# Kernel tuning notes

Hardware: AMD Instinct MI355X
Metric: run time of the kernel (lower is better)

## Reference

```python
import jax, jax.numpy as jnp
import numpy as np

B, T, HS, WS = 4, 16, 32, 64          # batch, time, lat, lon
D_MODEL, N_HEADS = 256, 8
E = D_MODEL // N_HEADS                 # 32 per-head dim
MODES = [8, 8, 16]
F_LAST = WS // 2 + 1                   # 33 rfft bins on last dim
M_LAST = MODES[-1]                     # 16 kept rfft bins
M_PANEL = MODES[0] * MODES[1]          # 64 kept (T,HS) panel modes


def _sym_indexes(shape):
    # faithful numpy port of get_symmetry_index_in_fft_pannel
    shape = np.array(shape)
    idx = np.stack([t.flatten() for t in np.meshgrid(*[range(s) for s in shape])])
    idx2 = (-idx) % shape[:, None]
    fftshift = (idx + shape[:, None] // 2) % shape[:, None]
    center = (shape[:, None] - 1) / 2
    order = np.argsort(np.linalg.norm(fftshift - center, axis=0))
    idx = idx[:, order]
    idx2 = idx2[:, order]
    return np.ravel_multi_index(idx, shape), np.ravel_multi_index(idx2, shape)


def _picked_panel():
    # lowest-frequency mode selection honoring Hermitian pairing
    i1, i2 = _sym_indexes((T, HS))
    picked = []
    for a, b in zip(i1, i2):
        if a in picked or b in picked:
            continue
        picked.append(a)
        if len(picked) == M_PANEL:
            break
    return np.array(picked, dtype=np.int32), i1.astype(np.int32), i2.astype(np.int32)


def setup_inputs() -> dict:
    key = jax.random.key(0)
    ks = jax.random.split(key, 12)
    sl = 1.0 / np.float32(np.sqrt(D_MODEL))
    sw = np.float32(0.02)
    panel, s1, s2 = _picked_panel()
    return {
        "x": jax.random.normal(ks[0], (B, T, HS, WS, D_MODEL), jnp.float32),
        "Wq": jax.random.normal(ks[1], (D_MODEL, D_MODEL), jnp.float32) * sl,
        "bq": jnp.zeros((D_MODEL,), jnp.float32),
        "Wk": jax.random.normal(ks[2], (D_MODEL, D_MODEL), jnp.float32) * sl,
        "bk": jnp.zeros((D_MODEL,), jnp.float32),
        "Wv": jax.random.normal(ks[3], (D_MODEL, D_MODEL), jnp.float32) * sl,
        "bv": jnp.zeros((D_MODEL,), jnp.float32),
        "Wo": jax.random.normal(ks[4], (D_MODEL, D_MODEL), jnp.float32) * sl,
        "bo": jnp.zeros((D_MODEL,), jnp.float32),
        "w_real": jax.random.normal(ks[5], (N_HEADS, E, E, M_PANEL, M_LAST), jnp.float32) * sw,
        "w_imag": jax.random.normal(ks[6], (N_HEADS, E, E, M_PANEL, M_LAST), jnp.float32) * sw,
        "panel_idx": jnp.asarray(panel),
        "sym_idx1": jnp.asarray(s1),
        "sym_idx2": jnp.asarray(s2),
    }


def reference(x, Wq, bq, Wk, bk, Wv, bv, Wo, bo, w_real, w_imag,
              panel_idx, sym_idx1, sym_idx2):
    # QKV projections (the torch layer computes all three; FourierBlockN uses q)
    q = (x @ Wq + bq).reshape(B, T, HS, WS, N_HEADS, E).transpose(0, 4, 5, 1, 2, 3)
    _k = (x @ Wk + bk)
    _v = (x @ Wv + bv)
    # rfftn over the spacetime dims -> (B,H,E,T,HS,F_LAST)
    x_ft = jnp.fft.rfftn(q, axes=(-3, -2, -1)).reshape(B, N_HEADS, E, T * HS, F_LAST)
    # gather selected frequency modes
    x_sel = x_ft[:, :, :, panel_idx, :M_LAST]                    # (B,H,E,Mp,Ml)
    w = w_real + 1j * w_imag                                      # (H,E,E,Mp,Ml)
    out_sel = jnp.einsum('bhipf,hiopf->bhopf', x_sel, w)
    out_ft = jnp.zeros_like(x_ft)
    out_ft = out_ft.at[:, :, :, panel_idx, :M_LAST].set(out_sel)
    # canonical_fft_freq: enforce Hermitian symmetry on the (T,HS) panel
    out_ft = out_ft.at[:, :, :, sym_idx1, :].set(
        (out_ft[:, :, :, sym_idx1, :] + jnp.conj(out_ft[:, :, :, sym_idx2, :])) * 0.5)
    out_ft = out_ft.reshape(B, N_HEADS, E, T, HS, F_LAST)
    o = jnp.fft.irfftn(out_ft, s=(T, HS, WS), axes=(-3, -2, -1))  # (B,H,E,T,HS,WS)
    o = o.transpose(0, 3, 4, 5, 1, 2).reshape(B, T, HS, WS, N_HEADS * E)
    return o @ Wo + bo
```

## Files before the change

kernel.cpp:

```cpp
#include <hip/hip_runtime.h>
#include <hip/hip_bf16.h>
#include <cmath>

#define BB 4
#define TT 16
#define HH 32
#define WW 64
#define DD 256
#define NHEAD 8
#define EE 32
#define MP 64
#define ML 16
#define SPAT 32768
#define S2D 512

constexpr size_t OFF_FTRE = 0;
constexpr size_t OFF_FTIM = 1024;
constexpr size_t OFF_FHRE = 2048;
constexpr size_t OFF_FHIM = 4096;
constexpr size_t OFF_CW   = 6144;
constexpr size_t OFF_W64I = 7168;
constexpr size_t OFF_W16  = 9216;
constexpr size_t OFF_FHT  = 9728;
constexpr size_t OFF_GB   = 16384;
constexpr size_t OFF_FW   = OFF_GB + 8388608;
constexpr size_t OFF_X    = OFF_FW + 16777216;
constexpr size_t OFF_V    = OFF_X + 2097152;
constexpr size_t OFF_WT   = OFF_V + 2097152;

typedef short short8 __attribute__((ext_vector_type(8)));
typedef float f32x4 __attribute__((ext_vector_type(4)));

static __device__ __forceinline__ unsigned short f2bf(float x) {
  union { float f; unsigned u; } v; v.f = x;
  unsigned r = v.u + 0x7fffu + ((v.u >> 16) & 1u);
  return (unsigned short)(r >> 16);
}

static __device__ __forceinline__ void gl_lds16(const void* g, void* l) {
  __builtin_amdgcn_global_load_lds((const __attribute__((address_space(1))) void*)g,
                                   (__attribute__((address_space(3))) void*)l, 16, 0, 0);
}

static __device__ __forceinline__ void xcd_tile_dg(int flat, int& tile, int& dg) {
  int w8 = flat >> 3, xl = flat & 7;
  tile = ((w8 >> 2) << 3) | xl;
  dg = w8 & 3;
}

__global__ __launch_bounds__(256) void k0_tables(const int* __restrict__ panel, float* __restrict__ tab) {
  __shared__ int kt[MP], kh[MP];
  int tid = threadIdx.x;
  if (tid < MP) { int s = panel[tid]; kt[tid] = s >> 5; kh[tid] = s & 31; }
  __syncthreads();
  const double PI2 = 6.283185307179586476925286766559;
  for (int i = tid; i < 1024; i += 256) {
    int p = i >> 4, t = i & 15;
    double a = -PI2 * (double)((t * kt[p]) & 15) / 16.0;
    tab[OFF_FTRE + i] = (float)cos(a);
    tab[OFF_FTIM + i] = (float)sin(a);
  }
  for (int i = tid; i < 2048; i += 256) {
    int p = i >> 5, hs = i & 31;
    double a = -PI2 * (double)((hs * kh[p]) & 31) / 32.0;
    tab[OFF_FHRE + i] = (float)cos(a);
    tab[OFF_FHIM + i] = (float)sin(a);
  }
  for (int i = tid; i < 1024; i += 256) {
    int f = i >> 6, wsx = i & 63;
    double a = PI2 * (double)((f * wsx) & 63) / 64.0;
    tab[OFF_CW + i] = (f == 0) ? (1.0f / 64.0f) : (float)(2.0 * cos(a) / 64.0);
  }
  for (int i = tid; i < 2048; i += 256) {
    int wsx = i >> 5, f2 = i & 31; int f = f2 >> 1;
    double a = -PI2 * (double)((wsx * f) & 63) / 64.0;
    tab[OFF_W64I + i] = (f2 & 1) ? (float)sin(a) : (float)cos(a);
  }
  if (tid < 256) {
    int t = tid >> 4, k = tid & 15;
    double a = -PI2 * (double)((t * k) & 15) / 16.0;
    tab[OFF_W16 + 2 * tid]     = (float)cos(a);
    tab[OFF_W16 + 2 * tid + 1] = (float)sin(a);
  }
  for (int i = tid; i < 2048; i += 256) {
    int hs = i >> 6, p = i & 63;
    double a = -PI2 * (double)((hs * kh[p]) & 31) / 32.0;
    tab[OFF_FHT + 2 * i]     = (float)cos(a);
    tab[OFF_FHT + 2 * i + 1] = (float)sin(a);
  }
}

__global__ __launch_bounds__(256) void conv_w(const float* __restrict__ Wq, const float* __restrict__ Wo,
                                              unsigned short* __restrict__ wqt, unsigned short* __restrict__ wot) {
  __shared__ float tile[32][33];
  const float* src = blockIdx.z ? Wo : Wq;
  unsigned short* dst = blockIdx.z ? wot : wqt;
  int k0 = blockIdx.x * 32, d0 = blockIdx.y * 32;
  int tx = threadIdx.x & 31, r4 = threadIdx.x >> 5;
  #pragma unroll
  for (int it = 0; it < 4; it++) {
    int row = r4 + it * 8;
    tile[row][tx] = src[(size_t)(k0 + row) * 256 + d0 + tx];
  }
  __syncthreads();
  #pragma unroll
  for (int it = 0; it < 4; it++) {
    int row = r4 + it * 8;
    dst[(size_t)(d0 + row) * 256 + k0 + tx] = f2bf(tile[tx][row]);
  }
}

__global__ __launch_bounds__(256) void k1f3(const float* __restrict__ x,
                                            const unsigned short* __restrict__ wqt,
                                            const float* __restrict__ bq,
                                            const float* __restrict__ tabp,
                                            float* __restrict__ Fwg) {
  __shared__ char smem[32768];
  char*  Al = smem;
  char*  Bl = smem + 16384;
  float* QL = (float*)smem;
  float* WL = (float*)(smem + 24576);
  int tile, dg;
  xcd_tile_dg(blockIdx.x, tile, dg);
  int d0 = dg << 6;
  int b = tile >> 8, st = tile & 255;
  int sp0 = st << 7;
  int tid = threadIdx.x;
  int lane = tid & 63, w = tid >> 6;
  int l15 = lane & 15, kg = lane >> 4;
  int swz = (l15 & 7) << 4;
  for (int i = tid; i < 2048; i += 256) WL[i] = tabp[OFF_W64I + i];
  f32x4 acc[2][4];
  #pragma unroll
  for (int mi = 0; mi < 2; mi++)
    #pragma unroll
    for (int ni = 0; ni < 4; ni++) acc[mi][ni] = (f32x4){0.f, 0.f, 0.f, 0.f};
  const float* xbase = x + ((size_t)b * 32768 + sp0) * 256;
  const char* Bbase = (const char*)(wqt + (size_t)d0 * 256);
  for (int k0 = 0; k0 < 256; k0 += 64) {
    #pragma unroll
    for (int it = 0; it < 2; it++) {
      int o = it * 4096 + tid * 16;
      int row = o >> 7, cb = o & 127;
      gl_lds16(Bbase + (size_t)row * 512 + k0 * 2 + (cb ^ ((row & 7) << 4)), Bl + o);
    }
    #pragma unroll
    for (int it = 0; it < 4; it++) {
      int idx = it * 256 + tid;
      int row = idx >> 3, g8 = idx & 7;
      const float* src = xbase + (size_t)row * 256 + k0 + g8 * 8;
      float4 a4 = *reinterpret_cast<const float4*>(src);
      float4 b4 = *reinterpret_cast<const float4*>(src + 4);
      short8 v;
      v[0] = (short)f2bf(a4.x); v[1] = (short)f2bf(a4.y); v[2] = (short)f2bf(a4.z); v[3] = (short)f2bf(a4.w);
      v[4] = (short)f2bf(b4.x); v[5] = (short)f2bf(b4.y); v[6] = (short)f2bf(b4.z); v[7] = (short)f2bf(b4.w);
      int byteoff = (row * 128 + g8 * 16) ^ ((row & 7) << 4);
      *reinterpret_cast<short8*>(Al + byteoff) = v;
    }
    __syncthreads();
    #pragma unroll
    for (int ks = 0; ks < 2; ks++) {
      int koff = (ks * 64 + kg * 16) ^ swz;
      short8 af[2], bfr[4];
      #pragma unroll
      for (int mi = 0; mi < 2; mi++)
        af[mi] = *reinterpret_cast<const short8*>(Al + (w * 32 + mi * 16 + l15) * 128 + koff);
      #pragma unroll
      for (int ni = 0; ni < 4; ni++)
        bfr[ni] = *reinterpret_cast<const short8*>(Bl + (ni * 16 + l15) * 128 + koff);
      #pragma unroll
      for (int mi = 0; mi < 2; mi++)
        #pragma unroll
        for (int ni = 0; ni < 4; ni++)
          acc[mi][ni] = __builtin_amdgcn_mfma_f32_16x16x32_bf16(af[mi], bfr[ni], acc[mi][ni], 0, 0, 0);
    }
    __syncthreads();
  }
  #pragma unroll
  for (int sh = 0; sh < 2; sh++) {
    if ((w >> 1) == sh) {
      #pragma unroll
      for (int ni = 0; ni < 4; ni++) {
        float bqv = bq[d0 + ni * 16 + l15];
        #pragma unroll
        for (int mi = 0; mi < 2; mi++) {
          f32x4 vv = acc[mi][ni];
          int m = (w & 1) * 32 + mi * 16 + kg * 4;
          #pragma unroll
          for (int j = 0; j < 4; j++)
            QL[(m + j) * 68 + ni * 16 + l15] = vv[j] + bqv;
        }
      }
    }
    __syncthreads();
    {
      int dp = tid >> 3, f2q = tid & 7;
      f32x4 a0 = (f32x4){0.f, 0.f, 0.f, 0.f};
      f32x4 a1 = (f32x4){0.f, 0.f, 0.f, 0.f};
      const float* qbase = QL + dp * 2;
      const float* wbase = WL + f2q * 4;
      #pragma unroll 8
      for (int wsx = 0; wsx < 64; wsx++) {
        float2 q = *reinterpret_cast<const float2*>(qbase + wsx * 68);
        f32x4 wv = *reinterpret_cast<const f32x4*>(wbase + wsx * 32);
        a0 += wv * q.x;
        a1 += wv * q.y;
      }
      int sgl = st * 2 + sh;
      size_t g0 = ((size_t)(b * 512 + sgl) * 256 + d0 + dp * 2) * 32 + f2q * 4;
      *reinterpret_cast<f32x4*>(&Fwg[g0]) = a0;
      *reinterpret_cast<f32x4*>(&Fwg[g0 + 32]) = a1;
    }
    if (sh == 0) __syncthreads();
  }
}

__global__ __launch_bounds__(512) void k3f(const float* __restrict__ Fwg, const float* __restrict__ tabp,
                                           const int* __restrict__ panel, float* __restrict__ X) {
  __shared__ float2 Floc[8192];
  __shared__ float2 fhT[32][64];
  __shared__ float2 W16L[16][16];
  __shared__ int ktl[64];
  int bd = blockIdx.x; int b = bd >> 8; int d = bd & 255;
  int tid = threadIdx.x;
  if (tid < 256) W16L[tid >> 4][tid & 15] = reinterpret_cast<const float2*>(tabp + OFF_W16)[tid];
  for (int i = tid; i < 2048; i += 512) fhT[i >> 6][i & 63] = reinterpret_cast<const float2*>(tabp + OFF_FHT)[i];
  if (tid < 64) ktl[tid] = panel[tid] >> 5;
  {
    const char* gb = (const char*)Fwg;
    #pragma unroll
    for (int r = 0; r < 8; r++) {
      int o = r * 8192 + tid * 16;
      int s = o >> 7; int c16 = (o >> 4) & 7;
      size_t gaddr = ((size_t)(b * 512 + s) * 256 + d) * 128 + (size_t)c16 * 16;
      gl_lds16(gb + gaddr, (char*)Floc + o);
    }
  }
  __syncthreads();
  int hs = tid >> 4, f = tid & 15;
  float2 v[16];
  #pragma unroll
  for (int t = 0; t < 16; t++) v[t] = Floc[(t * 32 + hs) * 16 + f];
  float2 a[16];
  #pragma unroll
  for (int k = 0; k < 16; k++) a[k] = make_float2(0.f, 0.f);
  #pragma unroll
  for (int t = 0; t < 16; t++) {
    float2 vv = v[t];
    #pragma unroll
    for (int k = 0; k < 16; k++) {
      float2 w = W16L[t][k];
      a[k].x += w.x * vv.x - w.y * vv.y;
      a[k].y += w.x * vv.y + w.y * vv.x;
    }
  }
  #pragma unroll
  for (int k = 0; k < 16; k++) Floc[(k * 32 + hs) * 16 + f] = a[k];
  __syncthreads();
  int p2 = tid >> 4;
  float2 res[2];
  #pragma unroll
  for (int half = 0; half < 2; half++) {
    int p = p2 + half * 32;
    int kt = ktl[p];
    float ar = 0.f, ai = 0.f;
    #pragma unroll 8
    for (int h = 0; h < 32; h++) {
      float2 e = fhT[h][p];
      float2 u = Floc[(kt * 32 + h) * 16 + f];
      ar += u.x * e.x - u.y * e.y;
      ai += u.x * e.y + u.y * e.x;
    }
    res[half] = make_float2(ar, ai);
  }
  float2* Xo = reinterpret_cast<float2*>(X) + (size_t)bd * 1024;
  Xo[p2 * 16 + f] = res[0];
  Xo[(p2 + 32) * 16 + f] = res[1];
}

__global__ __launch_bounds__(512) void k3b_mix(const float* __restrict__ X, const float* __restrict__ wreal,
                                               const float* __restrict__ wimag, float* __restrict__ V) {
  __shared__ float2 xs[4][32][16];
  int h = blockIdx.x >> 6;
  int p = blockIdx.x & 63;
  int tid = threadIdx.x;
  const float2* Xv = reinterpret_cast<const float2*>(X);
  for (int i = tid; i < 2048; i += 512) {
    int b = i >> 9, ii = (i >> 4) & 31, f = i & 15;
    xs[b][ii][f] = Xv[((size_t)(b * 256 + h * 32 + ii) * MP + p) * ML + f];
  }
  __syncthreads();
  int o = tid >> 4, f = tid & 15;
  float accr[4] = {0, 0, 0, 0}, acci[4] = {0, 0, 0, 0};
  for (int i = 0; i < 32; i++) {
    size_t wofs = ((((size_t)h * 32 + i) * 32 + o) * MP + p) * ML + f;
    float wr = wreal[wofs], wi = wimag[wofs];
    #pragma unroll
    for (int b = 0; b < 4; b++) {
      float2 xv = xs[b][i][f];
      accr[b] += xv.x * wr - xv.y * wi;
      acci[b] += xv.x * wi + xv.y * wr;
    }
  }
  #pragma unroll
  for (int b = 0; b < 4; b++)
    reinterpret_cast<float2*>(V)[((size_t)(b * 256 + h * 32 + o) * MP + p) * ML + f] =
        make_float2(accr[b], acci[b]);
}

__global__ __launch_bounds__(256) void k4a_inv(const float* __restrict__ V, const float* __restrict__ tabp,
                                               float* __restrict__ gbuf) {
  __shared__ float2 vl[64][16];
  __shared__ float2 ft[64][16];
  __shared__ float2 fh[64][32];
  int bd = blockIdx.x;
  int tid = threadIdx.x;
  const float2* Vv = reinterpret_cast<const float2*>(V) + (size_t)bd * MP * ML;
  for (int i = tid; i < 1024; i += 256) {
    vl[i >> 4][i & 15] = Vv[i];
    ft[i >> 4][i & 15] = make_float2(tabp[OFF_FTRE + i], tabp[OFF_FTIM + i]);
  }
  for (int i = tid; i < 2048; i += 256) fh[i >> 5][i & 31] = make_float2(tabp[OFF_FHRE + i], tabp[OFF_FHIM + i]);
  __syncthreads();
  float g0[16], g1[16];
  #pragma unroll
  for (int f = 0; f < 16; f++) { g0[f] = 0.f; g1[f] = 0.f; }
  int s0 = tid * 2;
  int t0 = s0 >> 5, hs0 = s0 & 31;
  int t1 = (s0 + 1) >> 5, hs1 = (s0 + 1) & 31;
  for (int p = 0; p < 64; p++) {
    float2 et0 = ft[p][t0], eh0 = fh[p][hs0];
    float2 et1 = ft[p][t1], eh1 = fh[p][hs1];
    float er0 = et0.x * eh0.x - et0.y * eh0.y;
    float ei0 = et0.x * eh0.y + et0.y * eh0.x;
    float er1 = et1.x * eh1.x - et1.y * eh1.y;
    float ei1 = et1.x * eh1.y + et1.y * eh1.x;
    #pragma unroll
    for (int f = 0; f < 16; f++) {
      float2 v = vl[p][f];
      g0[f] += v.x * er0 + v.y * ei0;
      g1[f] += v.x * er1 + v.y * ei1;
    }
  }
  float4* gb = reinterpret_cast<float4*>(gbuf + (size_t)bd * 8192 + (size_t)s0 * 16);
  #pragma unroll
  for (int q = 0; q < 4; q++)
    gb[q] = make_float4(g0[q * 4] * (1.f / 512.f), g0[q * 4 + 1] * (1.f / 512.f),
                        g0[q * 4 + 2] * (1.f / 512.f), g0[q * 4 + 3] * (1.f / 512.f));
  #pragma unroll
  for (int q = 0; q < 4; q++)
    gb[4 + q] = make_float4(g1[q * 4] * (1.f / 512.f), g1[q * 4 + 1] * (1.f / 512.f),
                            g1[q * 4 + 2] * (1.f / 512.f), g1[q * 4 + 3] * (1.f / 512.f));
}

__global__ __launch_bounds__(256) void k4b_cos(const float* __restrict__ gbuf, const float* __restrict__ tabp,
                                               unsigned short* __restrict__ ob) {
  __shared__ float Gs[256][17];
  __shared__ float cwL[16][64];
  int s = blockIdx.x, b = blockIdx.y;
  int tid = threadIdx.x;
  for (int i = tid; i < 4096; i += 256) {
    int c = i >> 4, f = i & 15;
    Gs[c][f] = gbuf[(size_t)(b * 256 + c) * 8192 + s * 16 + f];
  }
  for (int i = tid; i < 1024; i += 256) cwL[i >> 6][i & 63] = tabp[OFF_CW + i];
  __syncthreads();
  int c0 = (tid & 63) * 4, wsg = tid >> 6;
  float gv[4][16];
  #pragma unroll
  for (int j = 0; j < 4; j++)
    #pragma unroll
    for (int f = 0; f < 16; f++) gv[j][f] = Gs[c0 + j][f];
  for (int wsi = 0; wsi < 16; wsi++) {
    int wsx = wsg * 16 + wsi;
    float a0 = 0.f, a1 = 0.f, a2 = 0.f, a3 = 0.f;
    #pragma unroll
    for (int f = 0; f < 16; f++) {
      float cwv = cwL[f][wsx];
      a0 += gv[0][f] * cwv; a1 += gv[1][f] * cwv; a2 += gv[2][f] * cwv; a3 += gv[3][f] * cwv;
    }
    ushort4 u;
    u.x = f2bf(a0); u.y = f2bf(a1); u.z = f2bf(a2); u.w = f2bf(a3);
    *reinterpret_cast<ushort4*>(&ob[((size_t)b * SPAT + (size_t)s * 64 + wsx) * 256 + c0]) = u;
  }
}

__global__ __launch_bounds__(256) void k5_mfma(const unsigned short* __restrict__ ob,
                                               const unsigned short* __restrict__ wot,
                                               const float* __restrict__ bo, float* __restrict__ out) {
  __shared__ char smem[34816];
  unsigned short* Al = (unsigned short*)smem;
  unsigned short* Bl = (unsigned short*)(smem + 16384);
  float* OL = (float*)smem;
  int tile, dg;
  xcd_tile_dg(blockIdx.x, tile, dg);
  int b = tile >> 8, sp0 = (tile & 255) << 7, d0 = dg << 6;
  int tid = threadIdx.x;
  int lane = tid & 63, w = tid >> 6;
  int l15 = lane & 15, kg = lane >> 4;
  int swz = (l15 & 7) << 4;
  f32x4 acc[2][4];
  #pragma unroll
  for (int mi = 0; mi < 2; mi++)
    #pragma unroll
    for (int ni = 0; ni < 4; ni++) acc[mi][ni] = (f32x4){0.f, 0.f, 0.f, 0.f};
  const char* Abase = (const char*)(ob + ((size_t)b * 32768 + sp0) * 256);
  const char* Bbase = (const char*)(wot + (size_t)d0 * 256);
  for (int k0 = 0; k0 < 256; k0 += 64) {
    #pragma unroll
    for (int it = 0; it < 2; it++) {
      int o = tid * 16 + it * 4096 + 16384;
      int ol = o - 16384;
      int row = ol >> 7, cb = ol & 127;
      int scb = cb ^ ((row & 7) << 4);
      gl_lds16(Bbase + (size_t)row * 512 + k0 * 2 + scb, smem + o);
    }
    #pragma unroll
    for (int it = 0; it < 4; it++) {
      int o = tid * 16 + it * 4096;
      int row = o >> 7, cb = o & 127;
      int scb = cb ^ ((row & 7) << 4);
      gl_lds16(Abase + (size_t)row * 512 + k0 * 2 + scb, (char*)Al + o);
    }
    __syncthreads();
    #pragma unroll
    for (int ks = 0; ks < 2; ks++) {
      int koff = (ks * 64 + kg * 16) ^ swz;
      short8 af[2], bfr[4];
      #pragma unroll
      for (int mi = 0; mi < 2; mi++)
        af[mi] = *(const short8*)((const char*)Al + (w * 32 + mi * 16 + l15) * 128 + koff);
      #pragma unroll
      for (int ni = 0; ni < 4; ni++)
        bfr[ni] = *(const short8*)((const char*)Bl + (ni * 16 + l15) * 128 + koff);
      #pragma unroll
      for (int mi = 0; mi < 2; mi++)
        #pragma unroll
        for (int ni = 0; ni < 4; ni++)
          acc[mi][ni] = __builtin_amdgcn_mfma_f32_16x16x32_bf16(af[mi], bfr[ni], acc[mi][ni], 0, 0, 0);
    }
    __syncthreads();
  }
  #pragma unroll
  for (int ni = 0; ni < 4; ni++) {
    float bov = bo[d0 + ni * 16 + l15];
    #pragma unroll
    for (int mi = 0; mi < 2; mi++) {
      f32x4 v = acc[mi][ni];
      int m = w * 32 + mi * 16 + kg * 4;
      #pragma unroll
      for (int j = 0; j < 4; j++)
        OL[(m + j) * 68 + ni * 16 + l15] = v[j] + bov;
    }
  }
  __syncthreads();
  int f4 = tid & 15, r0 = tid >> 4;
  #pragma unroll
  for (int r = 0; r < 8; r++) {
    int m = r * 16 + r0;
    float4 val = *reinterpret_cast<const float4*>(&OL[m * 68 + f4 * 4]);
    *reinterpret_cast<float4*>(&out[((size_t)b * SPAT + sp0 + m) * 256 + d0 + f4 * 4]) = val;
  }
}

extern "C" void kernel_launch(void* const* d_in, const int* in_sizes, int n_in,
                              void* d_out, int out_size, void* d_ws, size_t ws_size,
                              hipStream_t stream) {
  const float* x  = (const float*)d_in[0];
  const float* Wq = (const float*)d_in[1];
  const float* bq = (const float*)d_in[2];
  const float* Wo = (const float*)d_in[7];
  const float* bo = (const float*)d_in[8];
  const float* wr = (const float*)d_in[9];
  const float* wi = (const float*)d_in[10];
  const int* panel = (const int*)d_in[11];
  float* wsf = (float*)d_ws;
  float* out = (float*)d_out;

  float*          gbuf = wsf + OFF_GB;
  unsigned short* obb  = (unsigned short*)(wsf + OFF_FW);
  unsigned short* wqt  = (unsigned short*)(wsf + OFF_WT);
  unsigned short* wot  = wqt + 65536;

  k0_tables<<<dim3(1), dim3(256), 0, stream>>>(panel, wsf);
  conv_w<<<dim3(8, 8, 2), dim3(256), 0, stream>>>(Wq, Wo, wqt, wot);
  k1f3<<<dim3(4096), dim3(256), 0, stream>>>(x, wqt, bq, wsf, wsf + OFF_FW);
  k3f<<<dim3(1024), dim3(512), 0, stream>>>(wsf + OFF_FW, wsf, panel, wsf + OFF_X);
  k3b_mix<<<dim3(512), dim3(512), 0, stream>>>(wsf + OFF_X, wr, wi, wsf + OFF_V);
  k4a_inv<<<dim3(1024), dim3(256), 0, stream>>>(wsf + OFF_V, wsf, gbuf);
  k4b_cos<<<dim3(512, 4), dim3(256), 0, stream>>>(gbuf, wsf, obb);
  k5_mfma<<<dim3(4096), dim3(256), 0, stream>>>(obb, wot, bo, out);
}
```

Baseline: 331.4 us.

## Preload full Wq slice to LDS and load A fragments directly from global

```diff
diff --git a/kernel.cpp b/kernel.cpp
--- a/kernel.cpp
+++ b/kernel.cpp
@@ -115,11 +115,10 @@
                                             const float* __restrict__ bq,
                                             const float* __restrict__ tabp,
                                             float* __restrict__ Fwg) {
-  __shared__ char smem[32768];
-  char*  Al = smem;
-  char*  Bl = smem + 16384;
+  __shared__ char smem[40960];
+  char*  Bl = smem;
   float* QL = (float*)smem;
-  float* WL = (float*)(smem + 24576);
+  float* WL = (float*)(smem + 32768);
   int tile, dg;
   xcd_tile_dg(blockIdx.x, tile, dg);
   int d0 = dg << 6;
@@ -130,52 +129,50 @@
   int l15 = lane & 15, kg = lane >> 4;
   int swz = (l15 & 7) << 4;
   for (int i = tid; i < 2048; i += 256) WL[i] = tabp[OFF_W64I + i];
+  {
+    const char* Bbase = (const char*)(wqt + (size_t)d0 * 256);
+    #pragma unroll
+    for (int it = 0; it < 8; it++) {
+      int o = it * 4096 + tid * 16;
+      int row = o >> 9, cb = o & 511;
+      gl_lds16(Bbase + (size_t)row * 512 + (cb ^ ((row & 7) << 4)), Bl + o);
+    }
+  }
+  __syncthreads();
   f32x4 acc[2][4];
   #pragma unroll
   for (int mi = 0; mi < 2; mi++)
     #pragma unroll
     for (int ni = 0; ni < 4; ni++) acc[mi][ni] = (f32x4){0.f, 0.f, 0.f, 0.f};
   const float* xbase = x + ((size_t)b * 32768 + sp0) * 256;
-  const char* Bbase = (const char*)(wqt + (size_t)d0 * 256);
   for (int k0 = 0; k0 < 256; k0 += 64) {
     #pragma unroll
-    for (int it = 0; it < 2; it++) {
-      int o = it * 4096 + tid * 16;
-      int row = o >> 7, cb = o & 127;
-      gl_lds16(Bbase + (size_t)row * 512 + k0 * 2 + (cb ^ ((row & 7) << 4)), Bl + o);
-    }
-    #pragma unroll
-    for (int it = 0; it < 4; it++) {
-      int idx = it * 256 + tid;
-      int row = idx >> 3, g8 = idx & 7;
-      const float* src = xbase + (size_t)row * 256 + k0 + g8 * 8;
-      float4 a4 = *reinterpret_cast<const float4*>(src);
-      float4 b4 = *reinterpret_cast<const float4*>(src + 4);
-      short8 v;
-      v[0] = (short)f2bf(a4.x); v[1] = (short)f2bf(a4.y); v[2] = (short)f2bf(a4.z); v[3] = (short)f2bf(a4.w);
-      v[4] = (short)f2bf(b4.x); v[5] = (short)f2bf(b4.y); v[6] = (short)f2bf(b4.z); v[7] = (short)f2bf(b4.w);
-      int byteoff = (row * 128 + g8 * 16) ^ ((row & 7) << 4);
-      *reinterpret_cast<short8*>(Al + byteoff) = v;
-    }
-    __syncthreads();
-    #pragma unroll
     for (int ks = 0; ks < 2; ks++) {
-      int koff = (ks * 64 + kg * 16) ^ swz;
-      short8 af[2], bfr[4];
-      #pragma unroll
-      for (int mi = 0; mi < 2; mi++)
-        af[mi] = *reinterpret_cast<const short8*>(Al + (w * 32 + mi * 16 + l15) * 128 + koff);
+      int ke = k0 + ks * 32 + kg * 8;
+      short8 af[2];
+      #pragma unroll
+      for (int mi = 0; mi < 2; mi++) {
+        const float* p = xbase + (size_t)(w * 32 + mi * 16 + l15) * 256 + ke;
+        float4 lo = *reinterpret_cast<const float4*>(p);
+        float4 hi = *reinterpret_cast<const float4*>(p + 4);
+        short8 v;
+        v[0] = (short)f2bf(lo.x); v[1] = (short)f2bf(lo.y); v[2] = (short)f2bf(lo.z); v[3] = (short)f2bf(lo.w);
+        v[4] = (short)f2bf(hi.x); v[5] = (short)f2bf(hi.y); v[6] = (short)f2bf(hi.z); v[7] = (short)f2bf(hi.w);
+        af[mi] = v;
+      }
+      int koff = (k0 * 2 + ks * 64 + kg * 16) ^ swz;
+      short8 bfr[4];
       #pragma unroll
       for (int ni = 0; ni < 4; ni++)
-        bfr[ni] = *reinterpret_cast<const short8*>(Bl + (ni * 16 + l15) * 128 + koff);
+        bfr[ni] = *reinterpret_cast<const short8*>(Bl + (size_t)(ni * 16 + l15) * 512 + koff);
       #pragma unroll
       for (int mi = 0; mi < 2; mi++)
         #pragma unroll
         for (int ni = 0; ni < 4; ni++)
           acc[mi][ni] = __builtin_amdgcn_mfma_f32_16x16x32_bf16(af[mi], bfr[ni], acc[mi][ni], 0, 0, 0);
     }
-    __syncthreads();
-  }
+  }
+  __syncthreads();
   #pragma unroll
   for (int sh = 0; sh < 2; sh++) {
     if ((w >> 1) == sh) {
```

Measured after the change: 361.2 us. 1.09x slower.

## Split k3f frequency dimension into two halves to halve LDS footprint

Applied to the files above, without the earlier changes.

```diff
diff --git a/kernel.cpp b/kernel.cpp
--- a/kernel.cpp
+++ b/kernel.cpp
@@ -217,7 +217,7 @@
 
 __global__ __launch_bounds__(512) void k3f(const float* __restrict__ Fwg, const float* __restrict__ tabp,
                                            const int* __restrict__ panel, float* __restrict__ X) {
-  __shared__ float2 Floc[8192];
+  __shared__ float2 Floc[4096];
   __shared__ float2 fhT[32][64];
   __shared__ float2 W16L[16][16];
   __shared__ int ktl[64];
@@ -226,56 +226,55 @@
   if (tid < 256) W16L[tid >> 4][tid & 15] = reinterpret_cast<const float2*>(tabp + OFF_W16)[tid];
   for (int i = tid; i < 2048; i += 512) fhT[i >> 6][i & 63] = reinterpret_cast<const float2*>(tabp + OFF_FHT)[i];
   if (tid < 64) ktl[tid] = panel[tid] >> 5;
-  {
-    const char* gb = (const char*)Fwg;
-    #pragma unroll
-    for (int r = 0; r < 8; r++) {
-      int o = r * 8192 + tid * 16;
-      int s = o >> 7; int c16 = (o >> 4) & 7;
-      size_t gaddr = ((size_t)(b * 512 + s) * 256 + d) * 128 + (size_t)c16 * 16;
-      gl_lds16(gb + gaddr, (char*)Floc + o);
-    }
-  }
-  __syncthreads();
-  int hs = tid >> 4, f = tid & 15;
-  float2 v[16];
-  #pragma unroll
-  for (int t = 0; t < 16; t++) v[t] = Floc[(t * 32 + hs) * 16 + f];
-  float2 a[16];
-  #pragma unroll
-  for (int k = 0; k < 16; k++) a[k] = make_float2(0.f, 0.f);
-  #pragma unroll
-  for (int t = 0; t < 16; t++) {
-    float2 vv = v[t];
-    #pragma unroll
-    for (int k = 0; k < 16; k++) {
-      float2 w = W16L[t][k];
-      a[k].x += w.x * vv.x - w.y * vv.y;
-      a[k].y += w.x * vv.y + w.y * vv.x;
-    }
-  }
-  #pragma unroll
-  for (int k = 0; k < 16; k++) Floc[(k * 32 + hs) * 16 + f] = a[k];
-  __syncthreads();
-  int p2 = tid >> 4;
-  float2 res[2];
-  #pragma unroll
-  for (int half = 0; half < 2; half++) {
-    int p = p2 + half * 32;
-    int kt = ktl[p];
-    float ar = 0.f, ai = 0.f;
-    #pragma unroll 8
-    for (int h = 0; h < 32; h++) {
-      float2 e = fhT[h][p];
-      float2 u = Floc[(kt * 32 + h) * 16 + f];
-      ar += u.x * e.x - u.y * e.y;
-      ai += u.x * e.y + u.y * e.x;
-    }
-    res[half] = make_float2(ar, ai);
-  }
-  float2* Xo = reinterpret_cast<float2*>(X) + (size_t)bd * 1024;
-  Xo[p2 * 16 + f] = res[0];
-  Xo[(p2 + 32) * 16 + f] = res[1];
+  #pragma unroll
+  for (int fh = 0; fh < 2; fh++) {
+    {
+      const char* gb = (const char*)Fwg;
+      #pragma unroll
+      for (int r = 0; r < 4; r++) {
+        int o = r * 8192 + tid * 16;
+        int s = o >> 6; int c16 = (o >> 4) & 3;
+        size_t gaddr = ((size_t)(b * 512 + s) * 256 + d) * 128 + (size_t)fh * 64 + (size_t)c16 * 16;
+        gl_lds16(gb + gaddr, (char*)Floc + o);
+      }
+    }
+    __syncthreads();
+    int f = tid & 7, hs = (tid >> 3) & 31, rep = tid >> 8;
+    float2 v[16];
+    #pragma unroll
+    for (int t = 0; t < 16; t++) v[t] = Floc[(t * 32 + hs) * 8 + f];
+    __syncthreads();
+    float2 a[8];
+    #pragma unroll
+    for (int k8 = 0; k8 < 8; k8++) a[k8] = make_float2(0.f, 0.f);
+    #pragma unroll
+    for (int t = 0; t < 16; t++) {
+      float2 vv = v[t];
+      #pragma unroll
+      for (int k8 = 0; k8 < 8; k8++) {
+        float2 w = W16L[t][rep * 8 + k8];
+        a[k8].x += w.x * vv.x - w.y * vv.y;
+        a[k8].y += w.x * vv.y + w.y * vv.x;
+      }
+    }
+    #pragma unroll
+    for (int k8 = 0; k8 < 8; k8++) Floc[((rep * 8 + k8) * 32 + hs) * 8 + f] = a[k8];
+    __syncthreads();
+    {
+      int p = tid >> 3, ff = tid & 7;
+      int kt = ktl[p];
+      float ar = 0.f, ai = 0.f;
+      #pragma unroll 8
+      for (int h = 0; h < 32; h++) {
+        float2 e = fhT[h][p];
+        float2 u = Floc[(kt * 32 + h) * 8 + ff];
+        ar += u.x * e.x - u.y * e.y;
+        ai += u.x * e.y + u.y * e.x;
+      }
+      reinterpret_cast<float2*>(X)[(size_t)bd * 1024 + p * 16 + fh * 8 + ff] = make_float2(ar, ai);
+    }
+    if (fh == 0) __syncthreads();
+  }
 }
 
 __global__ __launch_bounds__(512) void k3b_mix(const float* __restrict__ X, const float* __restrict__ wreal,
```

Measured after the change: 424.4 us. 1.28x slower.
